# Performance work log

Measured on AMD Instinct MI355X. Metric: run time of the kernel, lower is better.

Reference implementation:

```python
import jax, jax.numpy as jnp
import numpy as np


def setup_inputs() -> dict:
    key0 = jax.random.key(0)
    ks = jax.random.split(key0, 7)
    B, N, M, D, H = 2, 1024, 1024, 256, 128
    s = 1.0 / np.sqrt(D)
    return {
        "query": jax.random.normal(ks[0], (B, N, D), dtype=jnp.float32),
        "key": jax.random.normal(ks[1], (B, M, D), dtype=jnp.float32),
        "Wa_w": jax.random.normal(ks[2], (D, H), dtype=jnp.float32) * s,
        "Wa_b": jax.random.normal(ks[3], (H,), dtype=jnp.float32) * 0.02,
        "Wb_w": jax.random.normal(ks[4], (D, H), dtype=jnp.float32) * s,
        "Wb_b": jax.random.normal(ks[5], (H,), dtype=jnp.float32) * 0.02,
        "v_w": jax.random.normal(ks[6], (H,), dtype=jnp.float32) / np.sqrt(H),
    }


def reference(query, key, Wa_w, Wa_b, Wb_w, Wb_b, v_w):
    # a: [B,N,H], b: [B,M,H]
    a = query @ Wa_w + Wa_b
    b = key @ Wb_w + Wb_b
    # scores: tanh of broadcast add [B,N,M,H], contracted with v -> [B,N,M]
    scores = jnp.einsum("bnmh,h->bnm", jnp.tanh(a[:, :, None, :] + b[:, None, :, :]), v_w)
    attn = jax.nn.softmax(scores, axis=-1)
    # attended: [B,N,D]
    return jnp.einsum("bnm,bmd->bnd", attn, key)
```

## Files before the change

### kernel.cpp

```cpp
#include <hip/hip_runtime.h>
#include <hip/hip_fp16.h>

#define BB 2
#define NN 1024
#define MM 1024
#define DD 256
#define HH 128
#define C2LE 2.8853900817779268f
#define NEG2LOG2E -2.8853900817779268f
#define SHIFT_C -4.3280860f

typedef float v2f __attribute__((ext_vector_type(2)));
typedef float v4f __attribute__((ext_vector_type(4)));
typedef _Float16 h8 __attribute__((ext_vector_type(8)));

__global__ __launch_bounds__(256) void proj_conv_kernel(
    const float* __restrict__ query, const float* __restrict__ key,
    const float* __restrict__ Wa_w, const float* __restrict__ Wa_b,
    const float* __restrict__ Wb_w, const float* __restrict__ Wb_b,
    float* __restrict__ EaT, float* __restrict__ Eb,
    __half* __restrict__ KT_hi, __half* __restrict__ KT_lo) {
    __shared__ float rows[8][DD];
    __shared__ float partial[8][HH];
    __shared__ float t[64][65];
    const int tid = threadIdx.x;

    if (blockIdx.x >= 512) {
        const int cid = blockIdx.x - 512;
        const int m0 = (cid & 15) * 64, d0 = ((cid >> 4) & 3) * 64, b = cid >> 6;
        for (int i = tid; i < 1024; i += 256) {
            const int r = i >> 4, c4 = i & 15;
            const float4 v =
                *(const float4*)&key[((size_t)(b * MM + m0 + r)) * DD + d0 + c4 * 4];
            t[r][c4 * 4 + 0] = v.x; t[r][c4 * 4 + 1] = v.y;
            t[r][c4 * 4 + 2] = v.z; t[r][c4 * 4 + 3] = v.w;
        }
        __syncthreads();
        for (int i = tid; i < 4096; i += 256) {
            const int dr = i >> 6, mc = i & 63;
            const float f = t[mc][dr];
            const __half hi = __float2half(f);
            const __half lo = __float2half(f - __half2float(hi));
            const size_t o = ((size_t)(b * DD + d0 + dr)) * MM + m0 + mc;
            KT_hi[o] = hi;
            KT_lo[o] = lo;
        }
        return;
    }

    const int rb = blockIdx.x * 8;
    const bool isA = rb < BB * NN;
    const float* in = isA ? query : key;
    const float* W  = isA ? Wa_w : Wb_w;
    const float* bias = isA ? Wa_b : Wb_b;
    const int base = isA ? rb : rb - BB * NN;

    const float4* in4 = (const float4*)(in + (size_t)base * DD);
    float4* rows4 = (float4*)rows;
    rows4[tid] = in4[tid];
    rows4[tid + 256] = in4[tid + 256];
    __syncthreads();

    const int h = tid & 127, half = tid >> 7;
    const int d0 = half * 128;
    float acc[8] = {};
    for (int d = d0; d < d0 + 128; d += 4) {
        const float w0 = W[(d + 0) * HH + h];
        const float w1 = W[(d + 1) * HH + h];
        const float w2 = W[(d + 2) * HH + h];
        const float w3 = W[(d + 3) * HH + h];
#pragma unroll
        for (int r = 0; r < 8; ++r) {
            const float4 rv = *(const float4*)&rows[r][d];
            acc[r] = fmaf(rv.x, w0, fmaf(rv.y, w1, fmaf(rv.z, w2, fmaf(rv.w, w3, acc[r]))));
        }
    }
    if (half) {
#pragma unroll
        for (int r = 0; r < 8; ++r) partial[r][h] = acc[r];
    }
    __syncthreads();
    if (!half) {
        const float bv = bias[h];
        float ev[8];
#pragma unroll
        for (int r = 0; r < 8; ++r)
            ev[r] = __builtin_amdgcn_exp2f(C2LE * (acc[r] + partial[r][h] + bv));
        if (isA) {
            const int bq = base >> 10, nb = base & (NN - 1);
            float* dst = EaT + ((size_t)(bq * HH + h)) * NN + nb;
            *(float4*)dst = *(float4*)&ev[0];
            *(float4*)(dst + 4) = *(float4*)&ev[4];
        } else {
#pragma unroll
            for (int r = 0; r < 8; ++r)
                Eb[(size_t)(base + r) * HH + h] = ev[r];
        }
    }
}

__global__ __launch_bounds__(256) void scores_kernel(
    const float* __restrict__ EaT, const float* __restrict__ Eb,
    const float* __restrict__ v_w, __half* __restrict__ Ph,
    float* __restrict__ psum) {
    __shared__ float b_s[128 * 64];
    __shared__ float a_s[64 * 32];
    const int tid = threadIdx.x;
    const int m0 = blockIdx.x * 128, n0 = blockIdx.y * 32, b = blockIdx.z;
    const int lane = tid & 63;
    const int ng = __builtin_amdgcn_readfirstlane(threadIdx.x >> 6);
    const int skey = lane & 15;

    v2f acc[2][4] = {};
    for (int hc = 0; hc < 2; ++hc) {
        __syncthreads();
        for (int i = tid; i < 128 * 16; i += 256) {
            const int r = i >> 4, h4 = i & 15;
            *(float4*)&b_s[r * 64 + ((h4 ^ (r & 15)) << 2)] =
                *(const float4*)&Eb[((size_t)(b * MM + m0 + r)) * HH + hc * 64 + h4 * 4];
        }
        for (int i = tid; i < 64 * 8; i += 256) {
            const int hh = i >> 3, n4 = i & 7;
            *(float4*)&a_s[hh * 32 + n4 * 4] =
                *(const float4*)&EaT[((size_t)(b * HH + hc * 64 + hh)) * NN + n0 + n4 * 4];
        }
        __syncthreads();

#pragma unroll 4
        for (int h4 = 0; h4 < 16; ++h4) {
            const float4 w4 = *(const float4*)&v_w[hc * 64 + h4 * 4];
            const float* ap = &a_s[h4 * 4 * 32 + ng * 8];
            v2f A0[4], A1[4], A2[4], A3[4];
#pragma unroll
            for (int np = 0; np < 4; ++np) {
                A0[np] = *(const v2f*)&ap[0 * 32 + np * 2];
                A1[np] = *(const v2f*)&ap[1 * 32 + np * 2];
                A2[np] = *(const v2f*)&ap[2 * 32 + np * 2];
                A3[np] = *(const v2f*)&ap[3 * 32 + np * 2];
            }
#pragma unroll
            for (int mt = 0; mt < 2; ++mt) {
                const float4 b4 = *(const float4*)
                    &b_s[(mt * 64 + lane) * 64 + ((h4 ^ skey) << 2)];
#pragma unroll
                for (int np = 0; np < 4; ++np) {
                    const v2f u0 = A0[np] * b4.x + 1.0f;
                    const v2f u1 = A1[np] * b4.y + 1.0f;
                    const v2f u2 = A2[np] * b4.z + 1.0f;
                    const v2f u3 = A3[np] * b4.w + 1.0f;
                    const v2f p01 = u0 * u1, p23 = u2 * u3;
                    const v2f An = w4.x * u1 + w4.y * u0;
                    const v2f Bn = w4.z * u3 + w4.w * u2;
                    const v2f num = An * p23 + Bn * p01;
                    const v2f Pp = p01 * p23;
                    v2f r2;
                    r2.x = __builtin_amdgcn_rcpf(Pp.x);
                    r2.y = __builtin_amdgcn_rcpf(Pp.y);
                    acc[mt][np] = num * r2 + acc[mt][np];
                }
            }
        }
    }

    const size_t prow = ((size_t)b * NN + n0 + ng * 8) * MM + m0 + lane;
#pragma unroll
    for (int j = 0; j < 8; ++j) {
#pragma unroll
        for (int mt = 0; mt < 2; ++mt) {
            const float pv = __builtin_amdgcn_exp2f(
                fmaf(acc[mt][j >> 1][j & 1], NEG2LOG2E, SHIFT_C));
            Ph[prow + (size_t)j * MM + mt * 64] = __float2half(pv);
            float s = pv;
#pragma unroll
            for (int o = 32; o > 0; o >>= 1) s += __shfl_xor(s, o);
            if (lane == 0)
                psum[((size_t)(m0 / 64 + mt) * BB + b) * NN + n0 + ng * 8 + j] = s;
        }
    }
}

__global__ __launch_bounds__(512) void attend_kernel(
    const __half* __restrict__ Ph, const __half* __restrict__ KT_hi,
    const __half* __restrict__ KT_lo, float* __restrict__ partial) {
    __shared__ __align__(16) __half Ab[2][4096];
    __shared__ __align__(16) __half Bh[2][4096];
    __shared__ __align__(16) __half Bl[2][4096];

    const int bid = blockIdx.x;
    const int g = bid & 15, nt = bid >> 4;
    const int dt = g >> 2, ks = (g >> 1) & 1, b = g & 1;
    const int n0 = nt * 64, d0 = dt * 64, m0 = ks * 512;

    const int tid = threadIdx.x;
    const int lane = tid & 63;
    const int srow = tid & 15, skg = (tid >> 4) & 3;
    const int ssub = tid >> 6, skh = ssub & 1, st = ssub >> 1;
    const int scol = m0 + skh * 32 + skg * 8;

    const __half* srcA = Ph    + ((size_t)(b * NN + n0 + st * 16 + srow)) * MM + scol;
    const __half* srcH = KT_hi + ((size_t)(b * DD + d0 + st * 16 + srow)) * MM + scol;
    const __half* srcL = KT_lo + ((size_t)(b * DD + d0 + st * 16 + srow)) * MM + scol;

    const int wave = __builtin_amdgcn_readfirstlane(threadIdx.x >> 6);
    const int t0 = (wave >> 2) * 2, td = wave & 3;

    v4f ch0 = {0.f, 0.f, 0.f, 0.f}, cl0 = ch0, ch1 = ch0, cl1 = ch0;

    h8 ra = *(const h8*)srcA;
    h8 rh = *(const h8*)srcH;
    h8 rl = *(const h8*)srcL;

    int cur = 0;
#pragma unroll 1
    for (int step = 0; step < 8; ++step) {
        *(h8*)&Ab[cur][tid * 8] = ra;
        *(h8*)&Bh[cur][tid * 8] = rh;
        *(h8*)&Bl[cur][tid * 8] = rl;
        if (step < 7) {
            ra = *(const h8*)(srcA + (step + 1) * 64);
            rh = *(const h8*)(srcH + (step + 1) * 64);
            rl = *(const h8*)(srcL + (step + 1) * 64);
        }
        __syncthreads();
        const __half* A = Ab[cur];
        const __half* H = Bh[cur];
        const __half* L = Bl[cur];
        const h8 a00 = *(const h8*)&A[((t0 * 2 + 0) * 64 + lane) * 8];
        const h8 a01 = *(const h8*)&A[((t0 * 2 + 1) * 64 + lane) * 8];
        const h8 a10 = *(const h8*)&A[((t0 * 2 + 2) * 64 + lane) * 8];
        const h8 a11 = *(const h8*)&A[((t0 * 2 + 3) * 64 + lane) * 8];
        const h8 bh0 = *(const h8*)&H[((td * 2 + 0) * 64 + lane) * 8];
        const h8 bh1 = *(const h8*)&H[((td * 2 + 1) * 64 + lane) * 8];
        const h8 bl0 = *(const h8*)&L[((td * 2 + 0) * 64 + lane) * 8];
        const h8 bl1 = *(const h8*)&L[((td * 2 + 1) * 64 + lane) * 8];
        ch0 = __builtin_amdgcn_mfma_f32_16x16x32_f16(a00, bh0, ch0, 0, 0, 0);
        ch0 = __builtin_amdgcn_mfma_f32_16x16x32_f16(a01, bh1, ch0, 0, 0, 0);
        cl0 = __builtin_amdgcn_mfma_f32_16x16x32_f16(a00, bl0, cl0, 0, 0, 0);
        cl0 = __builtin_amdgcn_mfma_f32_16x16x32_f16(a01, bl1, cl0, 0, 0, 0);
        ch1 = __builtin_amdgcn_mfma_f32_16x16x32_f16(a10, bh0, ch1, 0, 0, 0);
        ch1 = __builtin_amdgcn_mfma_f32_16x16x32_f16(a11, bh1, ch1, 0, 0, 0);
        cl1 = __builtin_amdgcn_mfma_f32_16x16x32_f16(a10, bl0, cl1, 0, 0, 0);
        cl1 = __builtin_amdgcn_mfma_f32_16x16x32_f16(a11, bl1, cl1, 0, 0, 0);
        cur ^= 1;
    }

    const int row16 = lane & 15, kg = lane >> 4;
    const v4f c0 = ch0 + cl0, c1 = ch1 + cl1;
    float* pp0 = partial +
        (((size_t)ks * BB + b) * NN + n0 + t0 * 16 + kg * 4) * DD + d0 + td * 16 + row16;
    float* pp1 = pp0 + (size_t)16 * DD;
#pragma unroll
    for (int r = 0; r < 4; ++r) pp0[(size_t)r * DD] = c0[r];
#pragma unroll
    for (int r = 0; r < 4; ++r) pp1[(size_t)r * DD] = c1[r];
}

__global__ __launch_bounds__(256) void combine_kernel(
    const float* __restrict__ partial, const float* __restrict__ psum,
    float* __restrict__ out) {
    const int n = blockIdx.x, b = blockIdx.y, d = threadIdx.x;
    float s = 0.f;
#pragma unroll
    for (int q = 0; q < 16; ++q)
        s += psum[((size_t)q * BB + b) * NN + n];
    const size_t off = ((size_t)b * NN + n) * DD + d;
    const float a = partial[off] + partial[(size_t)BB * NN * DD + off];
    out[off] = a * __builtin_amdgcn_rcpf(s);
}

extern "C" void kernel_launch(void* const* d_in, const int* in_sizes, int n_in,
                              void* d_out, int out_size, void* d_ws, size_t ws_size,
                              hipStream_t stream) {
    const float* query = (const float*)d_in[0];
    const float* key   = (const float*)d_in[1];
    const float* Wa_w  = (const float*)d_in[2];
    const float* Wa_b  = (const float*)d_in[3];
    const float* Wb_w  = (const float*)d_in[4];
    const float* Wb_b  = (const float*)d_in[5];
    const float* v_w   = (const float*)d_in[6];
    float* out = (float*)d_out;

    float* ws = (float*)d_ws;
    float* EaT  = ws;
    float* Eb   = EaT + BB * NN * HH;
    float* psum = Eb + BB * MM * HH;
    __half* Ph    = (__half*)(psum + 16 * BB * NN);
    __half* KT_hi = Ph + (size_t)BB * NN * MM;
    __half* KT_lo = KT_hi + (size_t)BB * DD * MM;
    float* partial = (float*)(KT_lo + (size_t)BB * DD * MM);

    proj_conv_kernel<<<dim3(512 + 128), dim3(256), 0, stream>>>(
        query, key, Wa_w, Wa_b, Wb_w, Wb_b, EaT, Eb, KT_hi, KT_lo);
    scores_kernel<<<dim3(MM / 128, NN / 32, BB), dim3(256), 0, stream>>>(
        EaT, Eb, v_w, Ph, psum);
    attend_kernel<<<dim3(256), dim3(512), 0, stream>>>(
        Ph, KT_hi, KT_lo, partial);
    combine_kernel<<<dim3(NN, BB), dim3(256), 0, stream>>>(
        partial, psum, out);
}
```

Baseline: 61.35 us.

## Drop fp16 lo-split of key, split attend K four ways with XCD-aware mapping

Removes the hi/lo fp16 split of the transposed key, so the attend kernel runs half as many MFMAs and loads half the B operand bytes. It also splits the M reduction four ways instead of two, doubling the grid to 512 blocks, and remaps block indices so each XCD handles contiguous n tiles. The full __syncthreads is replaced with an explicit lgkmcnt wait plus s_barrier, and combine now sums four partials. The cost is lower precision in the P·K product and more partial-output traffic in combine.

```diff
diff --git a/kernel.cpp b/kernel.cpp
--- a/kernel.cpp
+++ b/kernel.cpp
@@ -19,7 +19,7 @@
     const float* __restrict__ Wa_w, const float* __restrict__ Wa_b,
     const float* __restrict__ Wb_w, const float* __restrict__ Wb_b,
     float* __restrict__ EaT, float* __restrict__ Eb,
-    __half* __restrict__ KT_hi, __half* __restrict__ KT_lo) {
+    __half* __restrict__ KT_hi) {
     __shared__ float rows[8][DD];
     __shared__ float partial[8][HH];
     __shared__ float t[64][65];
@@ -38,12 +38,8 @@
         __syncthreads();
         for (int i = tid; i < 4096; i += 256) {
             const int dr = i >> 6, mc = i & 63;
-            const float f = t[mc][dr];
-            const __half hi = __float2half(f);
-            const __half lo = __float2half(f - __half2float(hi));
-            const size_t o = ((size_t)(b * DD + d0 + dr)) * MM + m0 + mc;
-            KT_hi[o] = hi;
-            KT_lo[o] = lo;
+            KT_hi[((size_t)(b * DD + d0 + dr)) * MM + m0 + mc] =
+                __float2half(t[mc][dr]);
         }
         return;
     }
@@ -181,15 +177,15 @@
 
 __global__ __launch_bounds__(512) void attend_kernel(
     const __half* __restrict__ Ph, const __half* __restrict__ KT_hi,
-    const __half* __restrict__ KT_lo, float* __restrict__ partial) {
+    float* __restrict__ partial) {
     __shared__ __align__(16) __half Ab[2][4096];
     __shared__ __align__(16) __half Bh[2][4096];
-    __shared__ __align__(16) __half Bl[2][4096];
 
     const int bid = blockIdx.x;
-    const int g = bid & 15, nt = bid >> 4;
-    const int dt = g >> 2, ks = (g >> 1) & 1, b = g & 1;
-    const int n0 = nt * 64, d0 = dt * 64, m0 = ks * 512;
+    const int xcd = bid & 7, idx = bid >> 3;
+    const int b = idx & 1, ks = (idx >> 1) & 3, dt = (idx >> 3) & 3;
+    const int nt = xcd * 2 + ((idx >> 5) & 1);
+    const int n0 = nt * 64, d0 = dt * 64, m0 = ks * 256;
 
     const int tid = threadIdx.x;
     const int lane = tid & 63;
@@ -198,54 +194,45 @@
     const int scol = m0 + skh * 32 + skg * 8;
 
     const __half* srcA = Ph    + ((size_t)(b * NN + n0 + st * 16 + srow)) * MM + scol;
-    const __half* srcH = KT_hi + ((size_t)(b * DD + d0 + st * 16 + srow)) * MM + scol;
-    const __half* srcL = KT_lo + ((size_t)(b * DD + d0 + st * 16 + srow)) * MM + scol;
+    const __half* srcB = KT_hi + ((size_t)(b * DD + d0 + st * 16 + srow)) * MM + scol;
 
     const int wave = __builtin_amdgcn_readfirstlane(threadIdx.x >> 6);
     const int t0 = (wave >> 2) * 2, td = wave & 3;
 
-    v4f ch0 = {0.f, 0.f, 0.f, 0.f}, cl0 = ch0, ch1 = ch0, cl1 = ch0;
+    v4f c0 = {0.f, 0.f, 0.f, 0.f}, c1 = c0;
 
     h8 ra = *(const h8*)srcA;
-    h8 rh = *(const h8*)srcH;
-    h8 rl = *(const h8*)srcL;
+    h8 rb = *(const h8*)srcB;
 
     int cur = 0;
 #pragma unroll 1
-    for (int step = 0; step < 8; ++step) {
+    for (int step = 0; step < 4; ++step) {
         *(h8*)&Ab[cur][tid * 8] = ra;
-        *(h8*)&Bh[cur][tid * 8] = rh;
-        *(h8*)&Bl[cur][tid * 8] = rl;
-        if (step < 7) {
+        *(h8*)&Bh[cur][tid * 8] = rb;
+        if (step < 3) {
             ra = *(const h8*)(srcA + (step + 1) * 64);
-            rh = *(const h8*)(srcH + (step + 1) * 64);
-            rl = *(const h8*)(srcL + (step + 1) * 64);
-        }
-        __syncthreads();
+            rb = *(const h8*)(srcB + (step + 1) * 64);
+        }
+        asm volatile("s_waitcnt lgkmcnt(0)" ::: "memory");
+        __builtin_amdgcn_sched_barrier(0);
+        __builtin_amdgcn_s_barrier();
+
         const __half* A = Ab[cur];
-        const __half* H = Bh[cur];
-        const __half* L = Bl[cur];
+        const __half* B = Bh[cur];
         const h8 a00 = *(const h8*)&A[((t0 * 2 + 0) * 64 + lane) * 8];
         const h8 a01 = *(const h8*)&A[((t0 * 2 + 1) * 64 + lane) * 8];
         const h8 a10 = *(const h8*)&A[((t0 * 2 + 2) * 64 + lane) * 8];
         const h8 a11 = *(const h8*)&A[((t0 * 2 + 3) * 64 + lane) * 8];
-        const h8 bh0 = *(const h8*)&H[((td * 2 + 0) * 64 + lane) * 8];
-        const h8 bh1 = *(const h8*)&H[((td * 2 + 1) * 64 + lane) * 8];
-        const h8 bl0 = *(const h8*)&L[((td * 2 + 0) * 64 + lane) * 8];
-        const h8 bl1 = *(const h8*)&L[((td * 2 + 1) * 64 + lane) * 8];
-        ch0 = __builtin_amdgcn_mfma_f32_16x16x32_f16(a00, bh0, ch0, 0, 0, 0);
-        ch0 = __builtin_amdgcn_mfma_f32_16x16x32_f16(a01, bh1, ch0, 0, 0, 0);
-        cl0 = __builtin_amdgcn_mfma_f32_16x16x32_f16(a00, bl0, cl0, 0, 0, 0);
-        cl0 = __builtin_amdgcn_mfma_f32_16x16x32_f16(a01, bl1, cl0, 0, 0, 0);
-        ch1 = __builtin_amdgcn_mfma_f32_16x16x32_f16(a10, bh0, ch1, 0, 0, 0);
-        ch1 = __builtin_amdgcn_mfma_f32_16x16x32_f16(a11, bh1, ch1, 0, 0, 0);
-        cl1 = __builtin_amdgcn_mfma_f32_16x16x32_f16(a10, bl0, cl1, 0, 0, 0);
-        cl1 = __builtin_amdgcn_mfma_f32_16x16x32_f16(a11, bl1, cl1, 0, 0, 0);
+        const h8 b0  = *(const h8*)&B[((td * 2 + 0) * 64 + lane) * 8];
+        const h8 b1  = *(const h8*)&B[((td * 2 + 1) * 64 + lane) * 8];
+        c0 = __builtin_amdgcn_mfma_f32_16x16x32_f16(a00, b0, c0, 0, 0, 0);
+        c0 = __builtin_amdgcn_mfma_f32_16x16x32_f16(a01, b1, c0, 0, 0, 0);
+        c1 = __builtin_amdgcn_mfma_f32_16x16x32_f16(a10, b0, c1, 0, 0, 0);
+        c1 = __builtin_amdgcn_mfma_f32_16x16x32_f16(a11, b1, c1, 0, 0, 0);
         cur ^= 1;
     }
 
     const int row16 = lane & 15, kg = lane >> 4;
-    const v4f c0 = ch0 + cl0, c1 = ch1 + cl1;
     float* pp0 = partial +
         (((size_t)ks * BB + b) * NN + n0 + t0 * 16 + kg * 4) * DD + d0 + td * 16 + row16;
     float* pp1 = pp0 + (size_t)16 * DD;
@@ -264,7 +251,10 @@
     for (int q = 0; q < 16; ++q)
         s += psum[((size_t)q * BB + b) * NN + n];
     const size_t off = ((size_t)b * NN + n) * DD + d;
-    const float a = partial[off] + partial[(size_t)BB * NN * DD + off];
+    float a = 0.f;
+#pragma unroll
+    for (int ks = 0; ks < 4; ++ks)
+        a += partial[((size_t)ks * BB) * NN * DD + off];
     out[off] = a * __builtin_amdgcn_rcpf(s);
 }
 
@@ -286,15 +276,14 @@
     float* psum = Eb + BB * MM * HH;
     __half* Ph    = (__half*)(psum + 16 * BB * NN);
     __half* KT_hi = Ph + (size_t)BB * NN * MM;
-    __half* KT_lo = KT_hi + (size_t)BB * DD * MM;
-    float* partial = (float*)(KT_lo + (size_t)BB * DD * MM);
+    float* partial = (float*)(KT_hi + (size_t)BB * DD * MM);
 
     proj_conv_kernel<<<dim3(512 + 128), dim3(256), 0, stream>>>(
-        query, key, Wa_w, Wa_b, Wb_w, Wb_b, EaT, Eb, KT_hi, KT_lo);
+        query, key, Wa_w, Wa_b, Wb_w, Wb_b, EaT, Eb, KT_hi);
     scores_kernel<<<dim3(MM / 128, NN / 32, BB), dim3(256), 0, stream>>>(
         EaT, Eb, v_w, Ph, psum);
-    attend_kernel<<<dim3(256), dim3(512), 0, stream>>>(
-        Ph, KT_hi, KT_lo, partial);
+    attend_kernel<<<dim3(512), dim3(512), 0, stream>>>(
+        Ph, KT_hi, partial);
     combine_kernel<<<dim3(NN, BB), dim3(256), 0, stream>>>(
         partial, psum, out);
 }
```

Measured after the change: 58.31 us. 1.05x faster.
